# Kernel optimization log

Hardware: AMD Instinct MI355X
Metric: run time of the kernel (lower is better)

The kernel has to match this reference:

```python
import jax, jax.numpy as jnp
import numpy as np

N, E, F, G = 50000, 800000, 64, 1024


def _init_linear(key, fan_in, fan_out):
    kw, kb = jax.random.split(key)
    s = 1.0 / np.sqrt(fan_in)
    W = jax.random.uniform(kw, (fan_in, fan_out), minval=-s, maxval=s, dtype=jnp.float32)
    b = jax.random.uniform(kb, (fan_out,), minval=-s, maxval=s, dtype=jnp.float32)
    return W, b


def setup_inputs() -> dict:
    key = jax.random.key(0)
    ks = jax.random.split(key, 12)
    x = jax.random.normal(ks[0], (N, F), dtype=jnp.float32)
    edge_indices = jax.random.randint(ks[1], (2, E), 0, N, dtype=jnp.int64)
    batch_mapping = jnp.sort(jax.random.randint(ks[2], (N,), 0, G, dtype=jnp.int64))
    temperature = 300.0 + 50.0 * jax.random.uniform(ks[3], (G,), dtype=jnp.float32)
    mean = jnp.float32(2.0)
    std = jnp.float32(1.5)
    Wg1, bg1 = _init_linear(ks[4], 64, 64)
    Wg2, bg2 = _init_linear(ks[5], 64, 64)
    Wg3, bg3 = _init_linear(ks[6], 64, 64)
    Wd1, bd1 = _init_linear(ks[7], 64, 256)
    Wd2, bd2 = _init_linear(ks[8], 256, 128)
    Wa, ba = _init_linear(ks[9], 128, 3)
    return dict(x=x, edge_indices=edge_indices, batch_mapping=batch_mapping,
                temperature=temperature, mean=mean, std=std,
                Wg1=Wg1, bg1=bg1, Wg2=Wg2, bg2=bg2, Wg3=Wg3, bg3=bg3,
                Wd1=Wd1, bd1=bd1, Wd2=Wd2, bd2=bd2, Wa=Wa, ba=ba)


def _gcn_conv(h, W, b, src, dst, dinv):
    # PyG GCNConv: out = D^{-1/2}(A+I)D^{-1/2} h W + b, deg incl. self-loop
    hW = h @ W                                    # [N, out]
    norm = dinv[src] * dinv[dst]                  # [E]
    msg = hW[src] * norm[:, None]                 # gather + scale (memory-bound)
    out = jax.ops.segment_sum(msg, dst, num_segments=N)
    out = out + hW * (dinv * dinv)[:, None]       # self-loop contribution
    return out + b


def reference(x, edge_indices, batch_mapping, temperature, mean, std,
              Wg1, bg1, Wg2, bg2, Wg3, bg3, Wd1, bd1, Wd2, bd2, Wa, ba):
    src, dst = edge_indices[0], edge_indices[1]
    # degree (incl. self-loop) computed once; same for all layers
    deg = jax.ops.segment_sum(jnp.ones((E,), x.dtype), dst, num_segments=N) + 1.0
    dinv = jax.lax.rsqrt(deg)
    h = jax.nn.relu(_gcn_conv(x, Wg1, bg1, src, dst, dinv))
    h = jax.nn.relu(_gcn_conv(h, Wg2, bg2, src, dst, dinv))
    h = jax.nn.relu(_gcn_conv(h, Wg3, bg3, src, dst, dinv))
    # global_add_pool over graphs, then activation
    g = jax.ops.segment_sum(h, batch_mapping, num_segments=G)
    g = jax.nn.relu(g)
    # dense head (dropout = identity at eval)
    g = jax.nn.relu(g @ Wd1 + bd1)
    g = jax.nn.relu(g @ Wd2 + bd2)
    coeff = g @ Wa + ba                           # [G, 3] Antoine A, B, C
    A, B, C = coeff[:, 0], coeff[:, 1], coeff[:, 2]
    log_P = A - B / (temperature + C)
    return (log_P - mean) / std
```

## Files before the change

kernel.cpp:

```cpp
#include <hip/hip_runtime.h>
#include <hip/hip_bf16.h>

#define NN 50000
#define EE 800000
#define GG 1024
#define DUMMY 65535
#define B1B 256
#define B1E (EE / B1B)
#define NBUK 391
#define BUKCAP 2560
#define CSTRIDE 3584

__device__ __forceinline__ float blo(unsigned u) { return __uint_as_float(u << 16); }
__device__ __forceinline__ float bhi(unsigned u) { return __uint_as_float(u & 0xffff0000u); }
__device__ __forceinline__ unsigned packbf(float a, float b) {
    unsigned ua = __float_as_uint(a); ua += 0x7fffu + ((ua >> 16) & 1u);
    unsigned ub = __float_as_uint(b); ub += 0x7fffu + ((ub >> 16) & 1u);
    return (ua >> 16) | (ub & 0xffff0000u);
}

__global__ __launch_bounds__(256) void k_hist(const int* __restrict__ dst,
                                              int* __restrict__ cntmat) {
    __shared__ int h[NBUK];
    int tid = threadIdx.x;
    for (int k = tid; k < NBUK; k += 256) h[k] = 0;
    __syncthreads();
    int e0 = blockIdx.x * B1E;
    for (int k = 0; k < (B1E + 255) / 256; ++k) {
        int j = k * 256 + tid;
        if (j < B1E) atomicAdd(&h[dst[e0 + j] >> 7], 1);
    }
    __syncthreads();
    for (int k = tid; k < NBUK; k += 256) cntmat[k * B1B + blockIdx.x] = h[k];
}

__global__ __launch_bounds__(256) void k_scanmat(const int* __restrict__ cntmat,
                                                 int* __restrict__ basemat,
                                                 int* __restrict__ buktot) {
    __shared__ int sh[256];
    int b = blockIdx.x, t = threadIdx.x;
    int v = cntmat[b * B1B + t];
    sh[t] = v;
    __syncthreads();
    int acc = v;
    for (int off = 1; off < 256; off <<= 1) {
        int add = (t >= off) ? sh[t - off] : 0;
        __syncthreads();
        acc += add;
        sh[t] = acc;
        __syncthreads();
    }
    basemat[b * B1B + t] = b * BUKCAP + acc - v;
    if (t == 255) buktot[b] = acc;
}

__global__ __launch_bounds__(256) void k_scatter(const int* __restrict__ src,
                                                 const int* __restrict__ dst,
                                                 const int* __restrict__ basemat,
                                                 unsigned* __restrict__ bdat) {
    __shared__ unsigned sdata[B1E];
    __shared__ int h512[512];
    __shared__ int hexcl[NBUK];
    __shared__ int hcur[NBUK];
    __shared__ int gbase[NBUK];
    int tid = threadIdx.x;
    int e0  = blockIdx.x * B1E;

    h512[tid] = 0; h512[tid + 256] = 0;
    __syncthreads();

    for (int k = 0; k < (B1E + 255) / 256; ++k) {
        int j = k * 256 + tid;
        if (j < B1E) atomicAdd(&h512[dst[e0 + j] >> 7], 1);
    }
    __syncthreads();

    for (int off = 1; off < 512; off <<= 1) {
        int v0 = (tid >= off) ? h512[tid - off] : 0;
        int v1 = (tid + 256 >= off) ? h512[tid + 256 - off] : 0;
        __syncthreads();
        h512[tid] += v0;
        h512[tid + 256] += v1;
        __syncthreads();
    }
    if (tid < NBUK) {
        int ex = tid ? h512[tid - 1] : 0;
        hexcl[tid] = ex; hcur[tid] = ex;
        gbase[tid] = basemat[tid * B1B + blockIdx.x];
    }
    if (tid + 256 < NBUK) {
        int b = tid + 256;
        int ex = h512[b - 1];
        hexcl[b] = ex; hcur[b] = ex;
        gbase[b] = basemat[b * B1B + blockIdx.x];
    }
    __syncthreads();

    for (int k = 0; k < (B1E + 255) / 256; ++k) {
        int j = k * 256 + tid;
        if (j < B1E) {
            int d = dst[e0 + j];
            int s = src[e0 + j];
            int pos = atomicAdd(&hcur[d >> 7], 1);
            sdata[pos] = ((unsigned)d << 16) | (unsigned)(s & 0xffff);
        }
    }
    __syncthreads();

    for (int k = 0; k < (B1E + 255) / 256; ++k) {
        int j = k * 256 + tid;
        if (j < B1E) {
            unsigned v = sdata[j];
            int b = v >> 23;
            int dest = gbase[b] + (j - hexcl[b]);
            if (dest < (b + 1) * BUKCAP) bdat[dest] = v;
        }
    }
}

__global__ __launch_bounds__(256) void k_fill(const unsigned* __restrict__ bdat,
                                              const int* __restrict__ buktot,
                                              unsigned short* __restrict__ csr16,
                                              int* __restrict__ rowbeg,
                                              int* __restrict__ rowlen,
                                              float* __restrict__ dinv) {
    __shared__ int sc[128];
    __shared__ int lcnt[128];
    __shared__ int lcur[128];
    int b = blockIdx.x;
    int tid = threadIdx.x;
    if (tid < 128) lcnt[tid] = 0;
    __syncthreads();

    int ne = min(buktot[b], BUKCAP);
    int base = b * BUKCAP;

    for (int k = tid; k < ne; k += 256)
        atomicAdd(&lcnt[(bdat[base + k] >> 16) & 127], 1);
    __syncthreads();

    int plen = 0, cntv = 0;
    if (tid < 128) {
        cntv = lcnt[tid];
        plen = (cntv + 7) & ~7;
        sc[tid] = plen;
    }
    __syncthreads();
    for (int off = 1; off < 128; off <<= 1) {
        int add = (tid < 128 && tid >= off) ? sc[tid - off] : 0;
        __syncthreads();
        if (tid < 128) sc[tid] += add;
        __syncthreads();
    }
    if (tid < 128) {
        int excl = sc[tid] - plen;
        lcur[tid] = excl;
        int d = b * 128 + tid;
        if (d < NN) {
            rowbeg[d] = b * CSTRIDE + excl;
            rowlen[d] = plen;
            dinv[d]   = rsqrtf((float)cntv + 1.0f);
        }
    }
    __syncthreads();

    int cbase = b * CSTRIDE;
    for (int k = tid; k < ne; k += 256) {
        unsigned v = bdat[base + k];
        int slot = atomicAdd(&lcur[(v >> 16) & 127], 1);
        if (slot < CSTRIDE) csr16[cbase + slot] = (unsigned short)(v & 0xffff);
    }
}

__global__ __launch_bounds__(256) void k_gemm1(const float* __restrict__ x,
                                               const float* __restrict__ W,
                                               const float* __restrict__ dinv,
                                               unsigned* __restrict__ hWs) {
    __shared__ float hl[64 * 65];
    int tid  = threadIdx.x;
    int base = blockIdx.x * 64;
    const float4* hg = (const float4*)x;
#pragma unroll
    for (int i = 0; i < 4; ++i) {
        int idx4 = tid + i * 256;
        int row  = idx4 >> 4;
        int c4   = idx4 & 15;
        float4 v = make_float4(0.f, 0.f, 0.f, 0.f);
        if (base + row < NN) v = hg[(size_t)(base + row) * 16 + c4];
        float* dp = &hl[row * 65 + c4 * 4];
        dp[0] = v.x; dp[1] = v.y; dp[2] = v.z; dp[3] = v.w;
    }
    __syncthreads();

    int col4 = tid & 15;
    int rp   = tid >> 4;
    float4 a0 = make_float4(0, 0, 0, 0), a1 = a0, a2 = a0, a3 = a0;
    const float4* W4 = (const float4*)W;
#pragma unroll 8
    for (int k = 0; k < 64; ++k) {
        float4 w = W4[k * 16 + col4];
        float h0 = hl[rp * 65 + k];
        float h1 = hl[(rp + 16) * 65 + k];
        float h2 = hl[(rp + 32) * 65 + k];
        float h3 = hl[(rp + 48) * 65 + k];
        a0.x = fmaf(h0, w.x, a0.x); a0.y = fmaf(h0, w.y, a0.y); a0.z = fmaf(h0, w.z, a0.z); a0.w = fmaf(h0, w.w, a0.w);
        a1.x = fmaf(h1, w.x, a1.x); a1.y = fmaf(h1, w.y, a1.y); a1.z = fmaf(h1, w.z, a1.z); a1.w = fmaf(h1, w.w, a1.w);
        a2.x = fmaf(h2, w.x, a2.x); a2.y = fmaf(h2, w.y, a2.y); a2.z = fmaf(h2, w.z, a2.z); a2.w = fmaf(h2, w.w, a2.w);
        a3.x = fmaf(h3, w.x, a3.x); a3.y = fmaf(h3, w.y, a3.y); a3.z = fmaf(h3, w.z, a3.z); a3.w = fmaf(h3, w.w, a3.w);
    }
    float4 accs[4] = {a0, a1, a2, a3};
#pragma unroll
    for (int r = 0; r < 4; ++r) {
        int row = base + rp + 16 * r;
        if (row < NN) {
            float s = dinv[row];
            ((uint2*)hWs)[(size_t)row * 16 + col4] =
                make_uint2(packbf(accs[r].x * s, accs[r].y * s),
                           packbf(accs[r].z * s, accs[r].w * s));
        }
    }
}

__device__ __forceinline__ void gather_row2(int i0, int i1, bool v1, int p, int half,
                                            const int* __restrict__ rowbeg,
                                            const int* __restrict__ rowlen,
                                            const unsigned short* __restrict__ csr16,
                                            const unsigned* __restrict__ hWs,
                                            float& a0, float& a1, float& b0, float& b1) {
    unsigned s0 = hWs[(size_t)i0 * 32 + p];
    unsigned s1 = hWs[(size_t)(v1 ? i1 : DUMMY) * 32 + p];
    a0 = half ? 0.f : blo(s0);
    a1 = half ? 0.f : bhi(s0);
    b0 = half ? 0.f : blo(s1);
    b1 = half ? 0.f : bhi(s1);
    int e0 = rowbeg[i0], e0e = e0 + rowlen[i0];
    int e1 = 0, e1e = 0;
    if (v1) { e1 = rowbeg[i1]; e1e = e1 + rowlen[i1]; }

    while (e0 < e0e && e1 < e1e) {
        int c0 = csr16[e0 + half];
        int c1 = csr16[e0 + half + 2];
        int c2 = csr16[e0 + half + 4];
        int c3 = csr16[e0 + half + 6];
        int d0 = csr16[e1 + half];
        int d1 = csr16[e1 + half + 2];
        int d2 = csr16[e1 + half + 4];
        int d3 = csr16[e1 + half + 6];
        unsigned u0 = hWs[(size_t)c0 * 32 + p];
        unsigned u1 = hWs[(size_t)c1 * 32 + p];
        unsigned u2 = hWs[(size_t)c2 * 32 + p];
        unsigned u3 = hWs[(size_t)c3 * 32 + p];
        unsigned w0 = hWs[(size_t)d0 * 32 + p];
        unsigned w1 = hWs[(size_t)d1 * 32 + p];
        unsigned w2 = hWs[(size_t)d2 * 32 + p];
        unsigned w3 = hWs[(size_t)d3 * 32 + p];
        a0 += (blo(u0) + blo(u1)) + (blo(u2) + blo(u3));
        a1 += (bhi(u0) + bhi(u1)) + (bhi(u2) + bhi(u3));
        b0 += (blo(w0) + blo(w1)) + (blo(w2) + blo(w3));
        b1 += (bhi(w0) + bhi(w1)) + (bhi(w2) + bhi(w3));
        e0 += 8; e1 += 8;
    }
    for (; e0 < e0e; e0 += 8) {
        int c0 = csr16[e0 + half];
        int c1 = csr16[e0 + half + 2];
        int c2 = csr16[e0 + half + 4];
        int c3 = csr16[e0 + half + 6];
        unsigned u0 = hWs[(size_t)c0 * 32 + p];
        unsigned u1 = hWs[(size_t)c1 * 32 + p];
        unsigned u2 = hWs[(size_t)c2 * 32 + p];
        unsigned u3 = hWs[(size_t)c3 * 32 + p];
        a0 += (blo(u0) + blo(u1)) + (blo(u2) + blo(u3));
        a1 += (bhi(u0) + bhi(u1)) + (bhi(u2) + bhi(u3));
    }
    for (; e1 < e1e; e1 += 8) {
        int d0 = csr16[e1 + half];
        int d1 = csr16[e1 + half + 2];
        int d2 = csr16[e1 + half + 4];
        int d3 = csr16[e1 + half + 6];
        unsigned w0 = hWs[(size_t)d0 * 32 + p];
        unsigned w1 = hWs[(size_t)d1 * 32 + p];
        unsigned w2 = hWs[(size_t)d2 * 32 + p];
        unsigned w3 = hWs[(size_t)d3 * 32 + p];
        b0 += (blo(w0) + blo(w1)) + (blo(w2) + blo(w3));
        b1 += (bhi(w0) + bhi(w1)) + (bhi(w2) + bhi(w3));
    }
}

__global__ __launch_bounds__(256) void k_fused(const int* __restrict__ rowbeg,
                                               const int* __restrict__ rowlen,
                                               const unsigned short* __restrict__ csr16,
                                               const unsigned* __restrict__ hWs_prev,
                                               const float* __restrict__ dinv,
                                               const float* __restrict__ bias,
                                               const float* __restrict__ Wn,
                                               unsigned* __restrict__ hWs_next, int n) {
    __shared__ float hl[32 * 65];
    int tid  = threadIdx.x;
    int base = blockIdx.x * 32;
    int wave = tid >> 6;
    int lane = tid & 63;
    int p    = lane & 31;
    int half = lane >> 5;

    for (int m = 0; m < 4; ++m) {
        int i0 = base + wave * 8 + 2 * m;
        if (i0 >= n) break;
        int  i1 = i0 + 1;
        bool v1 = (i1 < n);
        float a0, a1, b0, b1;
        gather_row2(i0, i1, v1, p, half, rowbeg, rowlen, csr16, hWs_prev, a0, a1, b0, b1);
        a0 += __shfl_xor(a0, 32);
        a1 += __shfl_xor(a1, 32);
        b0 += __shfl_xor(b0, 32);
        b1 += __shfl_xor(b1, 32);
        if (half == 0) {
            int   r0 = wave * 8 + 2 * m;
            float d0 = dinv[i0];
            hl[r0 * 65 + 2 * p]     = fmaxf(fmaf(d0, a0, bias[2 * p]), 0.f);
            hl[r0 * 65 + 2 * p + 1] = fmaxf(fmaf(d0, a1, bias[2 * p + 1]), 0.f);
            if (v1) {
                float d1 = dinv[i1];
                hl[(r0 + 1) * 65 + 2 * p]     = fmaxf(fmaf(d1, b0, bias[2 * p]), 0.f);
                hl[(r0 + 1) * 65 + 2 * p + 1] = fmaxf(fmaf(d1, b1, bias[2 * p + 1]), 0.f);
            }
        }
    }
    __syncthreads();

    int col4 = tid & 15;
    int r    = tid >> 4;
    float4 a0 = make_float4(0, 0, 0, 0), a1 = a0;
    const float4* W4 = (const float4*)Wn;
#pragma unroll 8
    for (int k = 0; k < 64; ++k) {
        float4 w = W4[k * 16 + col4];
        float h0 = hl[r * 65 + k];
        float h1 = hl[(r + 16) * 65 + k];
        a0.x = fmaf(h0, w.x, a0.x); a0.y = fmaf(h0, w.y, a0.y); a0.z = fmaf(h0, w.z, a0.z); a0.w = fmaf(h0, w.w, a0.w);
        a1.x = fmaf(h1, w.x, a1.x); a1.y = fmaf(h1, w.y, a1.y); a1.z = fmaf(h1, w.z, a1.z); a1.w = fmaf(h1, w.w, a1.w);
    }
    int row0 = base + r, row1 = base + r + 16;
    if (row0 < n) {
        float s = dinv[row0];
        ((uint2*)hWs_next)[(size_t)row0 * 16 + col4] =
            make_uint2(packbf(a0.x * s, a0.y * s), packbf(a0.z * s, a0.w * s));
    }
    if (row1 < n) {
        float s = dinv[row1];
        ((uint2*)hWs_next)[(size_t)row1 * 16 + col4] =
            make_uint2(packbf(a1.x * s, a1.y * s), packbf(a1.z * s, a1.w * s));
    }
}

__global__ __launch_bounds__(256) void k_gather3(const int* __restrict__ rowbeg,
                                                 const int* __restrict__ rowlen,
                                                 const unsigned short* __restrict__ csr16,
                                                 const unsigned* __restrict__ hWs,
                                                 const float* __restrict__ dinv,
                                                 const float* __restrict__ bias,
                                                 unsigned* __restrict__ out) {
    int gt   = blockIdx.x * 256 + threadIdx.x;
    int j    = gt >> 6;
    int lane = gt & 63;
    int p    = lane & 31;
    int half = lane >> 5;
    int i0 = 2 * j;
    if (i0 >= NN) return;
    int i1 = i0 + 1;

    float a0, a1, b0, b1;
    gather_row2(i0, i1, true, p, half, rowbeg, rowlen, csr16, hWs, a0, a1, b0, b1);
    a0 += __shfl_xor(a0, 32);
    a1 += __shfl_xor(a1, 32);
    b0 += __shfl_xor(b0, 32);
    b1 += __shfl_xor(b1, 32);
    if (half == 0) {
        float d0 = dinv[i0];
        float d1 = dinv[i1];
        float o0 = fmaxf(fmaf(d0, a0, bias[2 * p]), 0.f);
        float o1 = fmaxf(fmaf(d0, a1, bias[2 * p + 1]), 0.f);
        float o2 = fmaxf(fmaf(d1, b0, bias[2 * p]), 0.f);
        float o3 = fmaxf(fmaf(d1, b1, bias[2 * p + 1]), 0.f);
        out[(size_t)i0 * 32 + p] = packbf(o0, o1);
        out[(size_t)i1 * 32 + p] = packbf(o2, o3);
    }
}

__device__ __forceinline__ int lowbd(const int* a, int n, int key) {
    int lo = 0, hi = n;
    while (lo < hi) { int m = (lo + hi) >> 1; if (a[m] < key) lo = m + 1; else hi = m; }
    return lo;
}

__global__ __launch_bounds__(256) void k_pooldense(const unsigned* __restrict__ h3,
                                                   const int* __restrict__ batch,
                                                   const float* __restrict__ Wd1, const float* __restrict__ bd1,
                                                   const float* __restrict__ Wd2, const float* __restrict__ bd2,
                                                   const float* __restrict__ Wa,  const float* __restrict__ ba,
                                                   const float* __restrict__ temp,
                                                   const float* __restrict__ mean,
                                                   const float* __restrict__ stdv,
                                                   float* __restrict__ out) {
    __shared__ float red[8][64];
    __shared__ float gl[64];
    __shared__ float d1[256];
    __shared__ float d2[128];
    __shared__ float coef[3];
    int tid = threadIdx.x;
    int gid = blockIdx.x;

    int lo = lowbd(batch, NN, gid);
    int hi = lowbd(batch, NN, gid + 1);

    int f2 = tid & 31;
    int rc = tid >> 5;
    float s0 = 0.f, s1 = 0.f;
    for (int r = lo + rc; r < hi; r += 8) {
        unsigned v = h3[(size_t)r * 32 + f2];
        s0 += blo(v); s1 += bhi(v);
    }
    red[rc][2 * f2]     = s0;
    red[rc][2 * f2 + 1] = s1;
    __syncthreads();
    if (tid < 64) {
        float s = 0.f;
#pragma unroll
        for (int j = 0; j < 8; ++j) s += red[j][tid];
        gl[tid] = fmaxf(s, 0.f);
    }
    __syncthreads();

    float a = bd1[tid];
#pragma unroll 8
    for (int k = 0; k < 64; ++k) a = fmaf(gl[k], Wd1[k * 256 + tid], a);
    d1[tid] = fmaxf(a, 0.f);
    __syncthreads();

    if (tid < 128) {
        float a2 = bd2[tid];
#pragma unroll 8
        for (int k = 0; k < 256; ++k) a2 = fmaf(d1[k], Wd2[k * 128 + tid], a2);
        d2[tid] = fmaxf(a2, 0.f);
    }
    __syncthreads();

    if (tid < 3) {
        float c = ba[tid];
        for (int k = 0; k < 128; ++k) c = fmaf(d2[k], Wa[k * 3 + tid], c);
        coef[tid] = c;
    }
    __syncthreads();

    if (tid == 0) {
        float A = coef[0], B = coef[1], C = coef[2];
        float T = temp[gid];
        float logP = A - B / (T + C);
        out[gid] = (logP - mean[0]) / stdv[0];
    }
}

extern "C" void kernel_launch(void* const* d_in, const int* in_sizes, int n_in,
                              void* d_out, int out_size, void* d_ws, size_t ws_size,
                              hipStream_t stream) {
    (void)in_sizes; (void)n_in; (void)out_size; (void)ws_size;
    const float* x     = (const float*)d_in[0];
    const int*   edges = (const int*)d_in[1];
    const int*   batch = (const int*)d_in[2];
    const float* temp  = (const float*)d_in[3];
    const float* mean  = (const float*)d_in[4];
    const float* stdv  = (const float*)d_in[5];
    const float* Wg1 = (const float*)d_in[6];  const float* bg1 = (const float*)d_in[7];
    const float* Wg2 = (const float*)d_in[8];  const float* bg2 = (const float*)d_in[9];
    const float* Wg3 = (const float*)d_in[10]; const float* bg3 = (const float*)d_in[11];
    const float* Wd1 = (const float*)d_in[12]; const float* bd1 = (const float*)d_in[13];
    const float* Wd2 = (const float*)d_in[14]; const float* bd2 = (const float*)d_in[15];
    const float* Wa  = (const float*)d_in[16]; const float* ba  = (const float*)d_in[17];

    char* wsb = (char*)d_ws;
    unsigned* bufB = (unsigned*)wsb;
    unsigned* bufA = bufB + (size_t)65536 * 32;
    unsigned* bdat = bufA + (size_t)65536 * 32;
    int*      cntmat  = (int*)(bdat + (size_t)NBUK * BUKCAP);
    int*      basemat = cntmat + (size_t)NBUK * B1B;
    int*      buktot  = basemat + (size_t)NBUK * B1B;
    float*    dinv    = (float*)(buktot + NBUK);
    int*      rowbeg  = (int*)(dinv + NN);
    int*      rowlen  = rowbeg + NN;
    unsigned short* csr16 = (unsigned short*)(rowlen + NN);

    const int* srcIdx = edges;
    const int* dstIdx = edges + EE;

    hipMemsetAsync(csr16, 0xFF, (size_t)NBUK * CSTRIDE * sizeof(unsigned short), stream);
    hipMemsetAsync(bufB + (size_t)DUMMY * 32, 0, 128, stream);
    hipMemsetAsync(bufA + (size_t)DUMMY * 32, 0, 128, stream);
    k_hist<<<B1B, 256, 0, stream>>>(dstIdx, cntmat);
    k_scanmat<<<NBUK, 256, 0, stream>>>(cntmat, basemat, buktot);
    k_scatter<<<B1B, 256, 0, stream>>>(srcIdx, dstIdx, basemat, bdat);
    k_fill<<<NBUK, 256, 0, stream>>>(bdat, buktot, csr16, rowbeg, rowlen, dinv);

    const int GEMM_BLOCKS  = (NN + 63) / 64;
    const int FUSED_BLOCKS = (NN + 31) / 32;
    const int PAIR_BLOCKS  = (NN / 2 * 64 + 255) / 256;

    k_gemm1<<<GEMM_BLOCKS, 256, 0, stream>>>(x, Wg1, dinv, bufB);
    k_fused<<<FUSED_BLOCKS, 256, 0, stream>>>(rowbeg, rowlen, csr16, bufB, dinv, bg1, Wg2, bufA, NN);
    k_fused<<<FUSED_BLOCKS, 256, 0, stream>>>(rowbeg, rowlen, csr16, bufA, dinv, bg2, Wg3, bufB, NN);
    k_gather3<<<PAIR_BLOCKS, 256, 0, stream>>>(rowbeg, rowlen, csr16, bufB, dinv, bg3, bufA);
    k_pooldense<<<GG, 256, 0, stream>>>(bufA, batch, Wd1, bd1, Wd2, bd2, Wa, ba, temp, mean, stdv, (float*)d_out);
}
```

Before: 160.5 us.

## Merge histogram with first GEMM, apply dinv in fill, gather four rows per wave

The first-layer GEMM now runs inside the histogram kernel as extra blocks, so it no longer waits for the degree computation. The dinv scaling of the GEMM output moves into k_fill, which rescales the bf16 rows after computing degrees. The gather now processes four destination rows per wave instead of two, giving more independent loads in flight. The cost is a second bf16 rounding on layer-1 features, an extra read and write pass over that buffer, and more wasted dummy loads when row lengths differ.

```diff
diff --git a/kernel.cpp b/kernel.cpp
--- a/kernel.cpp
+++ b/kernel.cpp
@@ -19,166 +19,30 @@
     return (ua >> 16) | (ub & 0xffff0000u);
 }
 
-__global__ __launch_bounds__(256) void k_hist(const int* __restrict__ dst,
-                                              int* __restrict__ cntmat) {
-    __shared__ int h[NBUK];
+__global__ __launch_bounds__(256) void k_histgemm(const int* __restrict__ dst,
+                                                  int* __restrict__ cntmat,
+                                                  const float* __restrict__ x,
+                                                  const float* __restrict__ W,
+                                                  unsigned* __restrict__ hWs,
+                                                  int histBlocks) {
+    __shared__ float hl[64 * 65];
     int tid = threadIdx.x;
-    for (int k = tid; k < NBUK; k += 256) h[k] = 0;
-    __syncthreads();
-    int e0 = blockIdx.x * B1E;
-    for (int k = 0; k < (B1E + 255) / 256; ++k) {
-        int j = k * 256 + tid;
-        if (j < B1E) atomicAdd(&h[dst[e0 + j] >> 7], 1);
-    }
-    __syncthreads();
-    for (int k = tid; k < NBUK; k += 256) cntmat[k * B1B + blockIdx.x] = h[k];
-}
-
-__global__ __launch_bounds__(256) void k_scanmat(const int* __restrict__ cntmat,
-                                                 int* __restrict__ basemat,
-                                                 int* __restrict__ buktot) {
-    __shared__ int sh[256];
-    int b = blockIdx.x, t = threadIdx.x;
-    int v = cntmat[b * B1B + t];
-    sh[t] = v;
-    __syncthreads();
-    int acc = v;
-    for (int off = 1; off < 256; off <<= 1) {
-        int add = (t >= off) ? sh[t - off] : 0;
-        __syncthreads();
-        acc += add;
-        sh[t] = acc;
-        __syncthreads();
-    }
-    basemat[b * B1B + t] = b * BUKCAP + acc - v;
-    if (t == 255) buktot[b] = acc;
-}
-
-__global__ __launch_bounds__(256) void k_scatter(const int* __restrict__ src,
-                                                 const int* __restrict__ dst,
-                                                 const int* __restrict__ basemat,
-                                                 unsigned* __restrict__ bdat) {
-    __shared__ unsigned sdata[B1E];
-    __shared__ int h512[512];
-    __shared__ int hexcl[NBUK];
-    __shared__ int hcur[NBUK];
-    __shared__ int gbase[NBUK];
-    int tid = threadIdx.x;
-    int e0  = blockIdx.x * B1E;
-
-    h512[tid] = 0; h512[tid + 256] = 0;
-    __syncthreads();
-
-    for (int k = 0; k < (B1E + 255) / 256; ++k) {
-        int j = k * 256 + tid;
-        if (j < B1E) atomicAdd(&h512[dst[e0 + j] >> 7], 1);
-    }
-    __syncthreads();
-
-    for (int off = 1; off < 512; off <<= 1) {
-        int v0 = (tid >= off) ? h512[tid - off] : 0;
-        int v1 = (tid + 256 >= off) ? h512[tid + 256 - off] : 0;
-        __syncthreads();
-        h512[tid] += v0;
-        h512[tid + 256] += v1;
-        __syncthreads();
-    }
-    if (tid < NBUK) {
-        int ex = tid ? h512[tid - 1] : 0;
-        hexcl[tid] = ex; hcur[tid] = ex;
-        gbase[tid] = basemat[tid * B1B + blockIdx.x];
-    }
-    if (tid + 256 < NBUK) {
-        int b = tid + 256;
-        int ex = h512[b - 1];
-        hexcl[b] = ex; hcur[b] = ex;
-        gbase[b] = basemat[b * B1B + blockIdx.x];
-    }
-    __syncthreads();
-
-    for (int k = 0; k < (B1E + 255) / 256; ++k) {
-        int j = k * 256 + tid;
-        if (j < B1E) {
-            int d = dst[e0 + j];
-            int s = src[e0 + j];
-            int pos = atomicAdd(&hcur[d >> 7], 1);
-            sdata[pos] = ((unsigned)d << 16) | (unsigned)(s & 0xffff);
+
+    if ((int)blockIdx.x < histBlocks) {
+        __shared__ int h[NBUK];
+        for (int k = tid; k < NBUK; k += 256) h[k] = 0;
+        __syncthreads();
+        int e0 = blockIdx.x * B1E;
+        for (int k = 0; k < (B1E + 255) / 256; ++k) {
+            int j = k * 256 + tid;
+            if (j < B1E) atomicAdd(&h[dst[e0 + j] >> 7], 1);
         }
-    }
-    __syncthreads();
-
-    for (int k = 0; k < (B1E + 255) / 256; ++k) {
-        int j = k * 256 + tid;
-        if (j < B1E) {
-            unsigned v = sdata[j];
-            int b = v >> 23;
-            int dest = gbase[b] + (j - hexcl[b]);
-            if (dest < (b + 1) * BUKCAP) bdat[dest] = v;
-        }
-    }
-}
-
-__global__ __launch_bounds__(256) void k_fill(const unsigned* __restrict__ bdat,
-                                              const int* __restrict__ buktot,
-                                              unsigned short* __restrict__ csr16,
-                                              int* __restrict__ rowbeg,
-                                              int* __restrict__ rowlen,
-                                              float* __restrict__ dinv) {
-    __shared__ int sc[128];
-    __shared__ int lcnt[128];
-    __shared__ int lcur[128];
-    int b = blockIdx.x;
-    int tid = threadIdx.x;
-    if (tid < 128) lcnt[tid] = 0;
-    __syncthreads();
-
-    int ne = min(buktot[b], BUKCAP);
-    int base = b * BUKCAP;
-
-    for (int k = tid; k < ne; k += 256)
-        atomicAdd(&lcnt[(bdat[base + k] >> 16) & 127], 1);
-    __syncthreads();
-
-    int plen = 0, cntv = 0;
-    if (tid < 128) {
-        cntv = lcnt[tid];
-        plen = (cntv + 7) & ~7;
-        sc[tid] = plen;
-    }
-    __syncthreads();
-    for (int off = 1; off < 128; off <<= 1) {
-        int add = (tid < 128 && tid >= off) ? sc[tid - off] : 0;
-        __syncthreads();
-        if (tid < 128) sc[tid] += add;
-        __syncthreads();
-    }
-    if (tid < 128) {
-        int excl = sc[tid] - plen;
-        lcur[tid] = excl;
-        int d = b * 128 + tid;
-        if (d < NN) {
-            rowbeg[d] = b * CSTRIDE + excl;
-            rowlen[d] = plen;
-            dinv[d]   = rsqrtf((float)cntv + 1.0f);
-        }
-    }
-    __syncthreads();
-
-    int cbase = b * CSTRIDE;
-    for (int k = tid; k < ne; k += 256) {
-        unsigned v = bdat[base + k];
-        int slot = atomicAdd(&lcur[(v >> 16) & 127], 1);
-        if (slot < CSTRIDE) csr16[cbase + slot] = (unsigned short)(v & 0xffff);
-    }
-}
-
-__global__ __launch_bounds__(256) void k_gemm1(const float* __restrict__ x,
-                                               const float* __restrict__ W,
-                                               const float* __restrict__ dinv,
-                                               unsigned* __restrict__ hWs) {
-    __shared__ float hl[64 * 65];
-    int tid  = threadIdx.x;
-    int base = blockIdx.x * 64;
+        __syncthreads();
+        for (int k = tid; k < NBUK; k += 256) cntmat[k * B1B + blockIdx.x] = h[k];
+        return;
+    }
+
+    int base = (blockIdx.x - histBlocks) * 64;
     const float4* hg = (const float4*)x;
 #pragma unroll
     for (int i = 0; i < 4; ++i) {
@@ -213,76 +77,216 @@
     for (int r = 0; r < 4; ++r) {
         int row = base + rp + 16 * r;
         if (row < NN) {
-            float s = dinv[row];
             ((uint2*)hWs)[(size_t)row * 16 + col4] =
-                make_uint2(packbf(accs[r].x * s, accs[r].y * s),
-                           packbf(accs[r].z * s, accs[r].w * s));
+                make_uint2(packbf(accs[r].x, accs[r].y), packbf(accs[r].z, accs[r].w));
         }
     }
 }
 
-__device__ __forceinline__ void gather_row2(int i0, int i1, bool v1, int p, int half,
+__global__ __launch_bounds__(256) void k_scanmat(const int* __restrict__ cntmat,
+                                                 int* __restrict__ basemat,
+                                                 int* __restrict__ buktot) {
+    __shared__ int sh[256];
+    int b = blockIdx.x, t = threadIdx.x;
+    int v = cntmat[b * B1B + t];
+    sh[t] = v;
+    __syncthreads();
+    int acc = v;
+    for (int off = 1; off < 256; off <<= 1) {
+        int add = (t >= off) ? sh[t - off] : 0;
+        __syncthreads();
+        acc += add;
+        sh[t] = acc;
+        __syncthreads();
+    }
+    basemat[b * B1B + t] = b * BUKCAP + acc - v;
+    if (t == 255) buktot[b] = acc;
+}
+
+__global__ __launch_bounds__(256) void k_scatter(const int* __restrict__ src,
+                                                 const int* __restrict__ dst,
+                                                 const int* __restrict__ basemat,
+                                                 unsigned* __restrict__ bdat) {
+    __shared__ unsigned sdata[B1E];
+    __shared__ int h512[512];
+    __shared__ int hexcl[NBUK];
+    __shared__ int hcur[NBUK];
+    __shared__ int gbase[NBUK];
+    int tid = threadIdx.x;
+    int e0  = blockIdx.x * B1E;
+
+    h512[tid] = 0; h512[tid + 256] = 0;
+    __syncthreads();
+
+    for (int k = 0; k < (B1E + 255) / 256; ++k) {
+        int j = k * 256 + tid;
+        if (j < B1E) atomicAdd(&h512[dst[e0 + j] >> 7], 1);
+    }
+    __syncthreads();
+
+    for (int off = 1; off < 512; off <<= 1) {
+        int v0 = (tid >= off) ? h512[tid - off] : 0;
+        int v1 = (tid + 256 >= off) ? h512[tid + 256 - off] : 0;
+        __syncthreads();
+        h512[tid] += v0;
+        h512[tid + 256] += v1;
+        __syncthreads();
+    }
+    if (tid < NBUK) {
+        int ex = tid ? h512[tid - 1] : 0;
+        hexcl[tid] = ex; hcur[tid] = ex;
+        gbase[tid] = basemat[tid * B1B + blockIdx.x];
+    }
+    if (tid + 256 < NBUK) {
+        int b = tid + 256;
+        int ex = h512[b - 1];
+        hexcl[b] = ex; hcur[b] = ex;
+        gbase[b] = basemat[b * B1B + blockIdx.x];
+    }
+    __syncthreads();
+
+    for (int k = 0; k < (B1E + 255) / 256; ++k) {
+        int j = k * 256 + tid;
+        if (j < B1E) {
+            int d = dst[e0 + j];
+            int s = src[e0 + j];
+            int pos = atomicAdd(&hcur[d >> 7], 1);
+            sdata[pos] = ((unsigned)d << 16) | (unsigned)(s & 0xffff);
+        }
+    }
+    __syncthreads();
+
+    for (int k = 0; k < (B1E + 255) / 256; ++k) {
+        int j = k * 256 + tid;
+        if (j < B1E) {
+            unsigned v = sdata[j];
+            int b = v >> 23;
+            int dest = gbase[b] + (j - hexcl[b]);
+            if (dest < (b + 1) * BUKCAP) bdat[dest] = v;
+        }
+    }
+}
+
+__global__ __launch_bounds__(256) void k_fill(const unsigned* __restrict__ bdat,
+                                              const int* __restrict__ buktot,
+                                              unsigned short* __restrict__ csr16,
+                                              int* __restrict__ rowbeg,
+                                              int* __restrict__ rowlen,
+                                              float* __restrict__ dinv,
+                                              unsigned* __restrict__ hWs1) {
+    __shared__ int sc[128];
+    __shared__ int lcnt[128];
+    __shared__ int lcur[128];
+    __shared__ float sdnv[128];
+    int b = blockIdx.x;
+    int tid = threadIdx.x;
+    if (tid < 128) lcnt[tid] = 0;
+    __syncthreads();
+
+    int ne = min(buktot[b], BUKCAP);
+    int base = b * BUKCAP;
+
+    for (int k = tid; k < ne; k += 256)
+        atomicAdd(&lcnt[(bdat[base + k] >> 16) & 127], 1);
+    __syncthreads();
+
+    int plen = 0, cntv = 0;
+    if (tid < 128) {
+        cntv = lcnt[tid];
+        plen = (cntv + 7) & ~7;
+        sc[tid] = plen;
+    }
+    __syncthreads();
+    for (int off = 1; off < 128; off <<= 1) {
+        int add = (tid < 128 && tid >= off) ? sc[tid - off] : 0;
+        __syncthreads();
+        if (tid < 128) sc[tid] += add;
+        __syncthreads();
+    }
+    if (tid < 128) {
+        int excl = sc[tid] - plen;
+        lcur[tid] = excl;
+        float dv = rsqrtf((float)cntv + 1.0f);
+        sdnv[tid] = dv;
+        int d = b * 128 + tid;
+        if (d < NN) {
+            rowbeg[d] = b * CSTRIDE + excl;
+            rowlen[d] = plen;
+            dinv[d]   = dv;
+        }
+    }
+    __syncthreads();
+
+    int cbase = b * CSTRIDE;
+    for (int k = tid; k < ne; k += 256) {
+        unsigned v = bdat[base + k];
+        int slot = atomicAdd(&lcur[(v >> 16) & 127], 1);
+        if (slot < CSTRIDE) csr16[cbase + slot] = (unsigned short)(v & 0xffff);
+    }
+
+    int nrow = min(128, NN - b * 128);
+    for (int k = tid; k < nrow * 32; k += 256) {
+        int r = (k >> 5);
+        size_t idx = (size_t)(b * 128 + r) * 32 + (k & 31);
+        unsigned v = hWs1[idx];
+        float s = sdnv[r];
+        hWs1[idx] = packbf(blo(v) * s, bhi(v) * s);
+    }
+}
+
+__device__ __forceinline__ void gather_row4(int i0, int i1, int i2, int i3,
+                                            bool v0, bool v1, bool v2, bool v3,
+                                            int p, int half,
                                             const int* __restrict__ rowbeg,
                                             const int* __restrict__ rowlen,
                                             const unsigned short* __restrict__ csr16,
                                             const unsigned* __restrict__ hWs,
-                                            float& a0, float& a1, float& b0, float& b1) {
-    unsigned s0 = hWs[(size_t)i0 * 32 + p];
-    unsigned s1 = hWs[(size_t)(v1 ? i1 : DUMMY) * 32 + p];
-    a0 = half ? 0.f : blo(s0);
-    a1 = half ? 0.f : bhi(s0);
-    b0 = half ? 0.f : blo(s1);
-    b1 = half ? 0.f : bhi(s1);
-    int e0 = rowbeg[i0], e0e = e0 + rowlen[i0];
-    int e1 = 0, e1e = 0;
-    if (v1) { e1 = rowbeg[i1]; e1e = e1 + rowlen[i1]; }
-
-    while (e0 < e0e && e1 < e1e) {
-        int c0 = csr16[e0 + half];
-        int c1 = csr16[e0 + half + 2];
-        int c2 = csr16[e0 + half + 4];
-        int c3 = csr16[e0 + half + 6];
-        int d0 = csr16[e1 + half];
-        int d1 = csr16[e1 + half + 2];
-        int d2 = csr16[e1 + half + 4];
-        int d3 = csr16[e1 + half + 6];
-        unsigned u0 = hWs[(size_t)c0 * 32 + p];
-        unsigned u1 = hWs[(size_t)c1 * 32 + p];
-        unsigned u2 = hWs[(size_t)c2 * 32 + p];
-        unsigned u3 = hWs[(size_t)c3 * 32 + p];
-        unsigned w0 = hWs[(size_t)d0 * 32 + p];
-        unsigned w1 = hWs[(size_t)d1 * 32 + p];
-        unsigned w2 = hWs[(size_t)d2 * 32 + p];
-        unsigned w3 = hWs[(size_t)d3 * 32 + p];
-        a0 += (blo(u0) + blo(u1)) + (blo(u2) + blo(u3));
-        a1 += (bhi(u0) + bhi(u1)) + (bhi(u2) + bhi(u3));
-        b0 += (blo(w0) + blo(w1)) + (blo(w2) + blo(w3));
-        b1 += (bhi(w0) + bhi(w1)) + (bhi(w2) + bhi(w3));
-        e0 += 8; e1 += 8;
-    }
-    for (; e0 < e0e; e0 += 8) {
-        int c0 = csr16[e0 + half];
-        int c1 = csr16[e0 + half + 2];
-        int c2 = csr16[e0 + half + 4];
-        int c3 = csr16[e0 + half + 6];
-        unsigned u0 = hWs[(size_t)c0 * 32 + p];
-        unsigned u1 = hWs[(size_t)c1 * 32 + p];
-        unsigned u2 = hWs[(size_t)c2 * 32 + p];
-        unsigned u3 = hWs[(size_t)c3 * 32 + p];
-        a0 += (blo(u0) + blo(u1)) + (blo(u2) + blo(u3));
-        a1 += (bhi(u0) + bhi(u1)) + (bhi(u2) + bhi(u3));
-    }
-    for (; e1 < e1e; e1 += 8) {
-        int d0 = csr16[e1 + half];
-        int d1 = csr16[e1 + half + 2];
-        int d2 = csr16[e1 + half + 4];
-        int d3 = csr16[e1 + half + 6];
-        unsigned w0 = hWs[(size_t)d0 * 32 + p];
-        unsigned w1 = hWs[(size_t)d1 * 32 + p];
-        unsigned w2 = hWs[(size_t)d2 * 32 + p];
-        unsigned w3 = hWs[(size_t)d3 * 32 + p];
-        b0 += (blo(w0) + blo(w1)) + (blo(w2) + blo(w3));
-        b1 += (bhi(w0) + bhi(w1)) + (bhi(w2) + bhi(w3));
+                                            float& a0, float& a1, float& b0, float& b1,
+                                            float& c0, float& c1, float& d0, float& d1) {
+    unsigned sA = hWs[(size_t)(v0 ? i0 : DUMMY) * 32 + p];
+    unsigned sB = hWs[(size_t)(v1 ? i1 : DUMMY) * 32 + p];
+    unsigned sC = hWs[(size_t)(v2 ? i2 : DUMMY) * 32 + p];
+    unsigned sD = hWs[(size_t)(v3 ? i3 : DUMMY) * 32 + p];
+    a0 = half ? 0.f : blo(sA); a1 = half ? 0.f : bhi(sA);
+    b0 = half ? 0.f : blo(sB); b1 = half ? 0.f : bhi(sB);
+    c0 = half ? 0.f : blo(sC); c1 = half ? 0.f : bhi(sC);
+    d0 = half ? 0.f : blo(sD); d1 = half ? 0.f : bhi(sD);
+
+    int eA = 0, eAe = 0, eB = 0, eBe = 0, eC = 0, eCe = 0, eD = 0, eDe = 0;
+    if (v0) { eA = rowbeg[i0]; eAe = eA + rowlen[i0]; }
+    if (v1) { eB = rowbeg[i1]; eBe = eB + rowlen[i1]; }
+    if (v2) { eC = rowbeg[i2]; eCe = eC + rowlen[i2]; }
+    if (v3) { eD = rowbeg[i3]; eDe = eD + rowlen[i3]; }
+
+    for (;;) {
+        bool aA = eA < eAe, aB = eB < eBe, aC = eC < eCe, aD = eD < eDe;
+        if (!(aA | aB | aC | aD)) break;
+        int oA = aA ? eA : 0, oB = aB ? eB : 0, oC = aC ? eC : 0, oD = aD ? eD : 0;
+        int iA0 = csr16[oA + half], iA1 = csr16[oA + half + 2], iA2 = csr16[oA + half + 4], iA3 = csr16[oA + half + 6];
+        int iB0 = csr16[oB + half], iB1 = csr16[oB + half + 2], iB2 = csr16[oB + half + 4], iB3 = csr16[oB + half + 6];
+        int iC0 = csr16[oC + half], iC1 = csr16[oC + half + 2], iC2 = csr16[oC + half + 4], iC3 = csr16[oC + half + 6];
+        int iD0 = csr16[oD + half], iD1 = csr16[oD + half + 2], iD2 = csr16[oD + half + 4], iD3 = csr16[oD + half + 6];
+        if (!aA) { iA0 = iA1 = iA2 = iA3 = DUMMY; }
+        if (!aB) { iB0 = iB1 = iB2 = iB3 = DUMMY; }
+        if (!aC) { iC0 = iC1 = iC2 = iC3 = DUMMY; }
+        if (!aD) { iD0 = iD1 = iD2 = iD3 = DUMMY; }
+        unsigned vA0 = hWs[(size_t)iA0 * 32 + p], vA1 = hWs[(size_t)iA1 * 32 + p];
+        unsigned vA2 = hWs[(size_t)iA2 * 32 + p], vA3 = hWs[(size_t)iA3 * 32 + p];
+        unsigned vB0 = hWs[(size_t)iB0 * 32 + p], vB1 = hWs[(size_t)iB1 * 32 + p];
+        unsigned vB2 = hWs[(size_t)iB2 * 32 + p], vB3 = hWs[(size_t)iB3 * 32 + p];
+        unsigned vC0 = hWs[(size_t)iC0 * 32 + p], vC1 = hWs[(size_t)iC1 * 32 + p];
+        unsigned vC2 = hWs[(size_t)iC2 * 32 + p], vC3 = hWs[(size_t)iC3 * 32 + p];
+        unsigned vD0 = hWs[(size_t)iD0 * 32 + p], vD1 = hWs[(size_t)iD1 * 32 + p];
+        unsigned vD2 = hWs[(size_t)iD2 * 32 + p], vD3 = hWs[(size_t)iD3 * 32 + p];
+        a0 += (blo(vA0) + blo(vA1)) + (blo(vA2) + blo(vA3));
+        a1 += (bhi(vA0) + bhi(vA1)) + (bhi(vA2) + bhi(vA3));
+        b0 += (blo(vB0) + blo(vB1)) + (blo(vB2) + blo(vB3));
+        b1 += (bhi(vB0) + bhi(vB1)) + (bhi(vB2) + bhi(vB3));
+        c0 += (blo(vC0) + blo(vC1)) + (blo(vC2) + blo(vC3));
+        c1 += (bhi(vC0) + bhi(vC1)) + (bhi(vC2) + bhi(vC3));
+        d0 += (blo(vD0) + blo(vD1)) + (blo(vD2) + blo(vD3));
+        d1 += (bhi(vD0) + bhi(vD1)) + (bhi(vD2) + bhi(vD3));
+        eA += aA ? 8 : 0; eB += aB ? 8 : 0; eC += aC ? 8 : 0; eD += aD ? 8 : 0;
     }
 }
 
@@ -302,26 +306,38 @@
     int p    = lane & 31;
     int half = lane >> 5;
 
-    for (int m = 0; m < 4; ++m) {
-        int i0 = base + wave * 8 + 2 * m;
+    for (int m = 0; m < 2; ++m) {
+        int i0 = base + wave * 8 + 4 * m;
         if (i0 >= n) break;
-        int  i1 = i0 + 1;
-        bool v1 = (i1 < n);
-        float a0, a1, b0, b1;
-        gather_row2(i0, i1, v1, p, half, rowbeg, rowlen, csr16, hWs_prev, a0, a1, b0, b1);
-        a0 += __shfl_xor(a0, 32);
-        a1 += __shfl_xor(a1, 32);
-        b0 += __shfl_xor(b0, 32);
-        b1 += __shfl_xor(b1, 32);
+        int i1 = i0 + 1, i2 = i0 + 2, i3 = i0 + 3;
+        bool v1 = i1 < n, v2 = i2 < n, v3 = i3 < n;
+        float a0, a1, b0, b1, c0, c1, d0, d1;
+        gather_row4(i0, i1, i2, i3, true, v1, v2, v3, p, half,
+                    rowbeg, rowlen, csr16, hWs_prev, a0, a1, b0, b1, c0, c1, d0, d1);
+        a0 += __shfl_xor(a0, 32); a1 += __shfl_xor(a1, 32);
+        b0 += __shfl_xor(b0, 32); b1 += __shfl_xor(b1, 32);
+        c0 += __shfl_xor(c0, 32); c1 += __shfl_xor(c1, 32);
+        d0 += __shfl_xor(d0, 32); d1 += __shfl_xor(d1, 32);
         if (half == 0) {
-            int   r0 = wave * 8 + 2 * m;
-            float d0 = dinv[i0];
-            hl[r0 * 65 + 2 * p]     = fmaxf(fmaf(d0, a0, bias[2 * p]), 0.f);
-            hl[r0 * 65 + 2 * p + 1] = fmaxf(fmaf(d0, a1, bias[2 * p + 1]), 0.f);
+            int r0 = wave * 8 + 4 * m;
+            float bb0 = bias[2 * p], bb1 = bias[2 * p + 1];
+            float dA = dinv[i0];
+            hl[r0 * 65 + 2 * p]     = fmaxf(fmaf(dA, a0, bb0), 0.f);
+            hl[r0 * 65 + 2 * p + 1] = fmaxf(fmaf(dA, a1, bb1), 0.f);
             if (v1) {
-                float d1 = dinv[i1];
-                hl[(r0 + 1) * 65 + 2 * p]     = fmaxf(fmaf(d1, b0, bias[2 * p]), 0.f);
-                hl[(r0 + 1) * 65 + 2 * p + 1] = fmaxf(fmaf(d1, b1, bias[2 * p + 1]), 0.f);
+                float dB = dinv[i1];
+                hl[(r0 + 1) * 65 + 2 * p]     = fmaxf(fmaf(dB, b0, bb0), 0.f);
+                hl[(r0 + 1) * 65 + 2 * p + 1] = fmaxf(fmaf(dB, b1, bb1), 0.f);
+            }
+            if (v2) {
+                float dC = dinv[i2];
+                hl[(r0 + 2) * 65 + 2 * p]     = fmaxf(fmaf(dC, c0, bb0), 0.f);
+                hl[(r0 + 2) * 65 + 2 * p + 1] = fmaxf(fmaf(dC, c1, bb1), 0.f);
+            }
+            if (v3) {
+                float dD = dinv[i3];
+                hl[(r0 + 3) * 65 + 2 * p]     = fmaxf(fmaf(dD, d0, bb0), 0.f);
+                hl[(r0 + 3) * 65 + 2 * p + 1] = fmaxf(fmaf(dD, d1, bb1), 0.f);
             }
         }
     }
@@ -360,29 +376,29 @@
                                                  const float* __restrict__ bias,
                                                  unsigned* __restrict__ out) {
     int gt   = blockIdx.x * 256 + threadIdx.x;
-    int j    = gt >> 6;
+    int q    = gt >> 6;
     int lane = gt & 63;
     int p    = lane & 31;
     int half = lane >> 5;
-    int i0 = 2 * j;
+    int i0 = 4 * q;
     if (i0 >= NN) return;
-    int i1 = i0 + 1;
-
-    float a0, a1, b0, b1;
-    gather_row2(i0, i1, true, p, half, rowbeg, rowlen, csr16, hWs, a0, a1, b0, b1);
-    a0 += __shfl_xor(a0, 32);
-    a1 += __shfl_xor(a1, 32);
-    b0 += __shfl_xor(b0, 32);
-    b1 += __shfl_xor(b1, 32);
+    int i1 = i0 + 1, i2 = i0 + 2, i3 = i0 + 3;
+
+    float a0, a1, b0, b1, c0, c1, d0, d1;
+    gather_row4(i0, i1, i2, i3, true, true, true, true, p, half,
+                rowbeg, rowlen, csr16, hWs, a0, a1, b0, b1, c0, c1, d0, d1);
+    a0 += __shfl_xor(a0, 32); a1 += __shfl_xor(a1, 32);
+    b0 += __shfl_xor(b0, 32); b1 += __shfl_xor(b1, 32);
+    c0 += __shfl_xor(c0, 32); c1 += __shfl_xor(c1, 32);
+    d0 += __shfl_xor(d0, 32); d1 += __shfl_xor(d1, 32);
+
     if (half == 0) {
-        float d0 = dinv[i0];
-        float d1 = dinv[i1];
-        float o0 = fmaxf(fmaf(d0, a0, bias[2 * p]), 0.f);
-        float o1 = fmaxf(fmaf(d0, a1, bias[2 * p + 1]), 0.f);
-        float o2 = fmaxf(fmaf(d1, b0, bias[2 * p]), 0.f);
-        float o3 = fmaxf(fmaf(d1, b1, bias[2 * p + 1]), 0.f);
-        out[(size_t)i0 * 32 + p] = packbf(o0, o1);
-        out[(size_t)i1 * 32 + p] = packbf(o2, o3);
+        float bb0 = bias[2 * p], bb1 = bias[2 * p + 1];
+        float dA = dinv[i0], dB = dinv[i1], dC = dinv[i2], dD = dinv[i3];
+        out[(size_t)i0 * 32 + p] = packbf(fmaxf(fmaf(dA, a0, bb0), 0.f), fmaxf(fmaf(dA, a1, bb1), 0.f));
+        out[(size_t)i1 * 32 + p] = packbf(fmaxf(fmaf(dB, b0, bb0), 0.f), fmaxf(fmaf(dB, b1, bb1), 0.f));
+        out[(size_t)i2 * 32 + p] = packbf(fmaxf(fmaf(dC, c0, bb0), 0.f), fmaxf(fmaf(dC, c1, bb1), 0.f));
+        out[(size_t)i3 * 32 + p] = packbf(fmaxf(fmaf(dD, d0, bb0), 0.f), fmaxf(fmaf(dD, d1, bb1), 0.f));
     }
 }
 
@@ -491,21 +507,20 @@
     const int* srcIdx = edges;
     const int* dstIdx = edges + EE;
 
+    const int GEMM_BLOCKS  = (NN + 63) / 64;
+    const int FUSED_BLOCKS = (NN + 31) / 32;
+    const int QUAD_BLOCKS  = (NN / 4 * 64 + 255) / 256;
+
     hipMemsetAsync(csr16, 0xFF, (size_t)NBUK * CSTRIDE * sizeof(unsigned short), stream);
     hipMemsetAsync(bufB + (size_t)DUMMY * 32, 0, 128, stream);
     hipMemsetAsync(bufA + (size_t)DUMMY * 32, 0, 128, stream);
-    k_hist<<<B1B, 256, 0, stream>>>(dstIdx, cntmat);
+    k_histgemm<<<B1B + GEMM_BLOCKS, 256, 0, stream>>>(dstIdx, cntmat, x, Wg1, bufB, B1B);
     k_scanmat<<<NBUK, 256, 0, stream>>>(cntmat, basemat, buktot);
     k_scatter<<<B1B, 256, 0, stream>>>(srcIdx, dstIdx, basemat, bdat);
-    k_fill<<<NBUK, 256, 0, stream>>>(bdat, buktot, csr16, rowbeg, rowlen, dinv);
-
-    const int GEMM_BLOCKS  = (NN + 63) / 64;
-    const int FUSED_BLOCKS = (NN + 31) / 32;
-    const int PAIR_BLOCKS  = (NN / 2 * 64 + 255) / 256;
-
-    k_gemm1<<<GEMM_BLOCKS, 256, 0, stream>>>(x, Wg1, dinv, bufB);
+    k_fill<<<NBUK, 256, 0, stream>>>(bdat, buktot, csr16, rowbeg, rowlen, dinv, bufB);
+
     k_fused<<<FUSED_BLOCKS, 256, 0, stream>>>(rowbeg, rowlen, csr16, bufB, dinv, bg1, Wg2, bufA, NN);
     k_fused<<<FUSED_BLOCKS, 256, 0, stream>>>(rowbeg, rowlen, csr16, bufA, dinv, bg2, Wg3, bufB, NN);
-    k_gather3<<<PAIR_BLOCKS, 256, 0, stream>>>(rowbeg, rowlen, csr16, bufB, dinv, bg3, bufA);
+    k_gather3<<<QUAD_BLOCKS, 256, 0, stream>>>(rowbeg, rowlen, csr16, bufB, dinv, bg3, bufA);
     k_pooldense<<<GG, 256, 0, stream>>>(bufA, batch, Wd1, bd1, Wd2, bd2, Wa, ba, temp, mean, stdv, (float*)d_out);
 }
```

Measured after the change: 159.8 us. Within noise of the previous version (-0.4%).
